# Optimization experiments

Hardware: AMD Instinct MI355X
Metric: run time of the kernel (lower is better)

Reference implementation:

```python
import jax, jax.numpy as jnp
import numpy as np
from jax import lax

B, D, H = 32768, 128, 256
N_ITER = 20


def setup_inputs() -> dict:
    key = jax.random.key(0)
    ks = jax.random.split(key, 7)
    return {
        "r": jax.random.normal(ks[0], (B, D), dtype=jnp.float32),
        "s": jax.random.normal(ks[1], (B, 1), dtype=jnp.float32),
        "pivot": jax.random.normal(ks[2], (D,), dtype=jnp.float32),
        "W1": jax.random.normal(ks[3], (D, H), dtype=jnp.float32) * 0.1,
        "b1": jax.random.normal(ks[4], (H,), dtype=jnp.float32) * 0.1,
        "w2": jax.random.normal(ks[5], (H,), dtype=jnp.float32) * 0.1,
        "b2": jax.random.normal(ks[6], (1,), dtype=jnp.float32) * 0.1,
        "n_iter": N_ITER,
    }


def _omega_step(x, W1, b1, w2, b2):
    # scalar implicit field omega evaluated on [B, D] points -> positive step in (0, 0.1)
    h = jnp.tanh(x @ W1 + b1)                      # [B, H]
    return 0.05 * (1.0 + jnp.tanh(h @ w2 + b2[0]))  # [B]


def reference(r, s, pivot, W1, b1, w2, b2, n_iter):
    # normalize ray directions; norm is detached in the original (stop_gradient)
    norm_of_x = jnp.linalg.norm(r, axis=1, keepdims=True)  # [B, 1]
    r_norm = r / lax.stop_gradient(norm_of_x)              # [B, D]

    # 20-step sphere-tracing-style ray marching along r_norm from pivot
    def step(alpha, _):
        x = pivot[None, :] + alpha[:, None] * r_norm       # [B, D]
        return alpha + _omega_step(x, W1, b1, w2, b2), None

    alpha0 = jnp.zeros((r.shape[0],), dtype=r.dtype)
    res_alpha, _ = lax.scan(step, alpha0, None, length=n_iter)  # [B]

    scale = jax.nn.sigmoid(s) * res_alpha[:, None]         # [B, 1]
    res_x = pivot[None, :] + scale * r_norm                # [B, D]
    return res_x
```

## Files before the change

### kernel.cpp

```cpp
#include <hip/hip_runtime.h>

#define DIM 128
#define HID 256
#define K2LE 2.885390081777927f
#define NTILES 16
#define RPW 16
#define WAVES 4
#define RPB (RPW * WAVES)
#define BFPAD 136

typedef __attribute__((ext_vector_type(8))) short bf16x8;
typedef __attribute__((ext_vector_type(4))) float f32x4;

__device__ __forceinline__ unsigned short f2bf(float f) {
    union { float f; unsigned u; } x; x.f = f;
    unsigned r = x.u + 0x7fffu + ((x.u >> 16) & 1u);
    return (unsigned short)(r >> 16);
}

__device__ __forceinline__ float sigmoid_fast(float x) {
    float t = __builtin_amdgcn_exp2f(-x * 1.4426950408889634f);
    return __builtin_amdgcn_rcpf(1.0f + t);
}

__global__ void k_prep(const float* __restrict__ pivot,
                       const float* __restrict__ W1,
                       const float* __restrict__ b1,
                       float* __restrict__ c2,
                       uint4* __restrict__ W1f) {
    const int tid = threadIdx.x;
    if (blockIdx.x == 0) {
        float a = b1[tid];
#pragma unroll 8
        for (int d = 0; d < DIM; ++d) a = fmaf(pivot[d], W1[d * HID + tid], a);
        c2[tid] = K2LE * a;
    }
    const int e  = blockIdx.x * 256 + tid;
    const int m  = e & 15;
    const int q  = (e >> 4) & 3;
    const int kk = (e >> 6) & 3;
    const int nt = e >> 8;
    const int n  = nt * 16 + m;
    const int k0 = kk * 32 + q * 8;
    unsigned w[4];
#pragma unroll
    for (int p = 0; p < 4; ++p) {
        unsigned lo = f2bf(W1[(k0 + 2 * p    ) * HID + n] * K2LE);
        unsigned hi = f2bf(W1[(k0 + 2 * p + 1) * HID + n] * K2LE);
        w[p] = lo | (hi << 16);
    }
    W1f[e] = make_uint4(w[0], w[1], w[2], w[3]);
}

__global__ __launch_bounds__(256, 2) void k_main(
    const float* __restrict__ r,
    const float* __restrict__ s,
    const float* __restrict__ pivot,
    const float* __restrict__ w2,
    const float* __restrict__ b2,
    const int* __restrict__ n_iter_p,
    const float* __restrict__ c2,
    const uint4* __restrict__ W1f,
    float* __restrict__ out)
{
    __shared__ unsigned short rnbf[RPB][BFPAD];
    __shared__ float alpha_s[WAVES][RPW];

    const int tid  = threadIdx.x;
    const int lane = tid & 63;
    const int wave = tid >> 6;
    const int m    = lane & 15;
    const int q    = lane >> 4;
    const int rowb = blockIdx.x * RPB + wave * RPW;
    const int n_iter = *n_iter_p;

    float2 rn2[RPW];
#pragma unroll 4
    for (int t = 0; t < RPW; ++t) {
        float2 v = *(const float2*)&r[(rowb + t) * DIM + lane * 2];
        float ss = v.x * v.x + v.y * v.y;
#pragma unroll
        for (int msk = 32; msk >= 1; msk >>= 1) ss += __shfl_xor(ss, msk, 64);
        float inv = __builtin_amdgcn_rsqf(ss);
        rn2[t].x = v.x * inv; rn2[t].y = v.y * inv;
        unsigned pack = (unsigned)f2bf(rn2[t].x) | ((unsigned)f2bf(rn2[t].y) << 16);
        *(unsigned*)&rnbf[wave * RPW + t][lane * 2] = pack;
    }

    bf16x8 afrag[4];
#pragma unroll
    for (int kk = 0; kk < 4; ++kk)
        afrag[kk] = *(const bf16x8*)&rnbf[wave * RPW + m][kk * 32 + q * 8];

    const bf16x8* __restrict__ wf = (const bf16x8*)W1f;
    const int fb = q * 16 + m;
    f32x4 acc[NTILES];
#pragma unroll
    for (int nt = 0; nt < NTILES; ++nt) {
        f32x4 a = {0.f, 0.f, 0.f, 0.f};
#pragma unroll
        for (int kk = 0; kk < 4; ++kk)
            a = __builtin_amdgcn_mfma_f32_16x16x32_bf16(
                    afrag[kk], wf[nt * 256 + kk * 64 + fb], a, 0, 0, 0);
        acc[nt] = a;
    }

    float w2f[NTILES], c2f[NTILES];
#pragma unroll
    for (int nt = 0; nt < NTILES; ++nt) {
        w2f[nt] = w2[nt * 16 + m];
        c2f[nt] = c2[nt * 16 + m];
    }
    float S = 0.f;
#pragma unroll
    for (int nt = 0; nt < NTILES; ++nt) S += w2f[nt];
#pragma unroll
    for (int msk = 1; msk <= 8; msk <<= 1) S += __shfl_xor(S, msk, 64);
    const float C0 = K2LE * (S + b2[0]);

    float alpha[4] = {0.f, 0.f, 0.f, 0.f};
    for (int it = 0; it < n_iter; ++it) {
        float part0 = 0.f, part1 = 0.f, part2 = 0.f, part3 = 0.f;
#pragma unroll
        for (int nt = 0; nt < NTILES; ++nt) {
            float u0 = __builtin_amdgcn_rcpf(__builtin_amdgcn_exp2f(fmaf(alpha[0], acc[nt][0], c2f[nt])) + 1.0f);
            float u1 = __builtin_amdgcn_rcpf(__builtin_amdgcn_exp2f(fmaf(alpha[1], acc[nt][1], c2f[nt])) + 1.0f);
            float u2 = __builtin_amdgcn_rcpf(__builtin_amdgcn_exp2f(fmaf(alpha[2], acc[nt][2], c2f[nt])) + 1.0f);
            float u3 = __builtin_amdgcn_rcpf(__builtin_amdgcn_exp2f(fmaf(alpha[3], acc[nt][3], c2f[nt])) + 1.0f);
            part0 = fmaf(w2f[nt], u0, part0);
            part1 = fmaf(w2f[nt], u1, part1);
            part2 = fmaf(w2f[nt], u2, part2);
            part3 = fmaf(w2f[nt], u3, part3);
        }
#pragma unroll
        for (int msk = 1; msk <= 8; msk <<= 1) {
            part0 += __shfl_xor(part0, msk, 64);
            part1 += __shfl_xor(part1, msk, 64);
            part2 += __shfl_xor(part2, msk, 64);
            part3 += __shfl_xor(part3, msk, 64);
        }
        float v0 = __builtin_amdgcn_rcpf(__builtin_amdgcn_exp2f(fmaf(-2.0f * K2LE, part0, C0)) + 1.0f);
        float v1 = __builtin_amdgcn_rcpf(__builtin_amdgcn_exp2f(fmaf(-2.0f * K2LE, part1, C0)) + 1.0f);
        float v2 = __builtin_amdgcn_rcpf(__builtin_amdgcn_exp2f(fmaf(-2.0f * K2LE, part2, C0)) + 1.0f);
        float v3 = __builtin_amdgcn_rcpf(__builtin_amdgcn_exp2f(fmaf(-2.0f * K2LE, part3, C0)) + 1.0f);
        alpha[0] += fmaf(-0.1f, v0, 0.1f);
        alpha[1] += fmaf(-0.1f, v1, 0.1f);
        alpha[2] += fmaf(-0.1f, v2, 0.1f);
        alpha[3] += fmaf(-0.1f, v3, 0.1f);
    }

    if (m == 0) {
#pragma unroll
        for (int rr = 0; rr < 4; ++rr) alpha_s[wave][q * 4 + rr] = alpha[rr];
    }
    __syncthreads();

    const float2 pv = *(const float2*)&pivot[lane * 2];
#pragma unroll 4
    for (int t = 0; t < RPW; ++t) {
        const int row = rowb + t;
        const float scale = sigmoid_fast(s[row]) * alpha_s[wave][t];
        float2 o;
        o.x = fmaf(scale, rn2[t].x, pv.x);
        o.y = fmaf(scale, rn2[t].y, pv.y);
        *(float2*)&out[row * DIM + lane * 2] = o;
    }
}

extern "C" void kernel_launch(void* const* d_in, const int* in_sizes, int n_in,
                              void* d_out, int out_size, void* d_ws, size_t ws_size,
                              hipStream_t stream) {
    const float* r      = (const float*)d_in[0];
    const float* s      = (const float*)d_in[1];
    const float* pivot  = (const float*)d_in[2];
    const float* W1     = (const float*)d_in[3];
    const float* b1     = (const float*)d_in[4];
    const float* w2     = (const float*)d_in[5];
    const float* b2     = (const float*)d_in[6];
    const int*   n_iter = (const int*)d_in[7];
    float* out = (float*)d_out;

    float* c2  = (float*)d_ws;
    uint4* W1f = (uint4*)((char*)d_ws + 4096);

    const int B = in_sizes[0] / DIM;

    k_prep<<<16, 256, 0, stream>>>(pivot, W1, b1, c2, W1f);
    k_main<<<B / RPB, 256, 0, stream>>>(r, s, pivot, w2, b2, n_iter, c2, W1f, out);
}
```

Measured before the change: 137.1 us.

## Split each 16-row tile across two waves to halve per-wave iteration work

Blocks now handle 32 rows instead of 64. Each pair of waves computes the same 16x256 MFMA tile, and each wave keeps only two of the four accumulator rows for the 20-step march. The normalized rays move from registers into a float LDS buffer, and launch bounds rise to 4 blocks per CU. The aim is to cut register pressure and the serial transcendental chain per wave, raising occupancy and latency hiding. The cost is duplicated MFMA work, extra LDS traffic and an added barrier.

New measurement: 137.5 us. No clear change (+0.2%).

```diff
diff --git a/kernel.cpp b/kernel.cpp
--- a/kernel.cpp
+++ b/kernel.cpp
@@ -4,9 +4,7 @@
 #define HID 256
 #define K2LE 2.885390081777927f
 #define NTILES 16
-#define RPW 16
-#define WAVES 4
-#define RPB (RPW * WAVES)
+#define RPB 32
 #define BFPAD 136
 
 typedef __attribute__((ext_vector_type(8))) short bf16x8;
@@ -52,7 +50,7 @@
     W1f[e] = make_uint4(w[0], w[1], w[2], w[3]);
 }
 
-__global__ __launch_bounds__(256, 2) void k_main(
+__global__ __launch_bounds__(256, 4) void k_main(
     const float* __restrict__ r,
     const float* __restrict__ s,
     const float* __restrict__ pivot,
@@ -64,37 +62,42 @@
     float* __restrict__ out)
 {
     __shared__ unsigned short rnbf[RPB][BFPAD];
-    __shared__ float alpha_s[WAVES][RPW];
+    __shared__ float rnf[RPB][DIM];
+    __shared__ float alpha_s[RPB];
 
     const int tid  = threadIdx.x;
     const int lane = tid & 63;
     const int wave = tid >> 6;
+    const int pr   = wave >> 1;
+    const int par  = wave & 1;
     const int m    = lane & 15;
     const int q    = lane >> 4;
-    const int rowb = blockIdx.x * RPB + wave * RPW;
+    const int rowblk = blockIdx.x * RPB;
     const int n_iter = *n_iter_p;
 
-    float2 rn2[RPW];
-#pragma unroll 4
-    for (int t = 0; t < RPW; ++t) {
-        float2 v = *(const float2*)&r[(rowb + t) * DIM + lane * 2];
+#pragma unroll
+    for (int t = 0; t < 8; ++t) {
+        const int lr = wave * 8 + t;
+        float2 v = *(const float2*)&r[(rowblk + lr) * DIM + lane * 2];
         float ss = v.x * v.x + v.y * v.y;
 #pragma unroll
         for (int msk = 32; msk >= 1; msk >>= 1) ss += __shfl_xor(ss, msk, 64);
         float inv = __builtin_amdgcn_rsqf(ss);
-        rn2[t].x = v.x * inv; rn2[t].y = v.y * inv;
-        unsigned pack = (unsigned)f2bf(rn2[t].x) | ((unsigned)f2bf(rn2[t].y) << 16);
-        *(unsigned*)&rnbf[wave * RPW + t][lane * 2] = pack;
+        float2 rn; rn.x = v.x * inv; rn.y = v.y * inv;
+        *(float2*)&rnf[lr][lane * 2] = rn;
+        unsigned pack = (unsigned)f2bf(rn.x) | ((unsigned)f2bf(rn.y) << 16);
+        *(unsigned*)&rnbf[lr][lane * 2] = pack;
     }
+    __syncthreads();
 
     bf16x8 afrag[4];
 #pragma unroll
     for (int kk = 0; kk < 4; ++kk)
-        afrag[kk] = *(const bf16x8*)&rnbf[wave * RPW + m][kk * 32 + q * 8];
+        afrag[kk] = *(const bf16x8*)&rnbf[pr * 16 + m][kk * 32 + q * 8];
 
     const bf16x8* __restrict__ wf = (const bf16x8*)W1f;
     const int fb = q * 16 + m;
-    f32x4 acc[NTILES];
+    float gA[NTILES], gB[NTILES];
 #pragma unroll
     for (int nt = 0; nt < NTILES; ++nt) {
         f32x4 a = {0.f, 0.f, 0.f, 0.f};
@@ -102,7 +105,8 @@
         for (int kk = 0; kk < 4; ++kk)
             a = __builtin_amdgcn_mfma_f32_16x16x32_bf16(
                     afrag[kk], wf[nt * 256 + kk * 64 + fb], a, 0, 0, 0);
-        acc[nt] = a;
+        gA[nt] = a[par * 2 + 0];
+        gB[nt] = a[par * 2 + 1];
     }
 
     float w2f[NTILES], c2f[NTILES];
@@ -118,51 +122,43 @@
     for (int msk = 1; msk <= 8; msk <<= 1) S += __shfl_xor(S, msk, 64);
     const float C0 = K2LE * (S + b2[0]);
 
-    float alpha[4] = {0.f, 0.f, 0.f, 0.f};
+    float alphaA = 0.f, alphaB = 0.f;
     for (int it = 0; it < n_iter; ++it) {
-        float part0 = 0.f, part1 = 0.f, part2 = 0.f, part3 = 0.f;
+        float pA = 0.f, pB = 0.f;
 #pragma unroll
         for (int nt = 0; nt < NTILES; ++nt) {
-            float u0 = __builtin_amdgcn_rcpf(__builtin_amdgcn_exp2f(fmaf(alpha[0], acc[nt][0], c2f[nt])) + 1.0f);
-            float u1 = __builtin_amdgcn_rcpf(__builtin_amdgcn_exp2f(fmaf(alpha[1], acc[nt][1], c2f[nt])) + 1.0f);
-            float u2 = __builtin_amdgcn_rcpf(__builtin_amdgcn_exp2f(fmaf(alpha[2], acc[nt][2], c2f[nt])) + 1.0f);
-            float u3 = __builtin_amdgcn_rcpf(__builtin_amdgcn_exp2f(fmaf(alpha[3], acc[nt][3], c2f[nt])) + 1.0f);
-            part0 = fmaf(w2f[nt], u0, part0);
-            part1 = fmaf(w2f[nt], u1, part1);
-            part2 = fmaf(w2f[nt], u2, part2);
-            part3 = fmaf(w2f[nt], u3, part3);
+            float uA = __builtin_amdgcn_rcpf(__builtin_amdgcn_exp2f(fmaf(alphaA, gA[nt], c2f[nt])) + 1.0f);
+            float uB = __builtin_amdgcn_rcpf(__builtin_amdgcn_exp2f(fmaf(alphaB, gB[nt], c2f[nt])) + 1.0f);
+            pA = fmaf(w2f[nt], uA, pA);
+            pB = fmaf(w2f[nt], uB, pB);
         }
 #pragma unroll
         for (int msk = 1; msk <= 8; msk <<= 1) {
-            part0 += __shfl_xor(part0, msk, 64);
-            part1 += __shfl_xor(part1, msk, 64);
-            part2 += __shfl_xor(part2, msk, 64);
-            part3 += __shfl_xor(part3, msk, 64);
+            pA += __shfl_xor(pA, msk, 64);
+            pB += __shfl_xor(pB, msk, 64);
         }
-        float v0 = __builtin_amdgcn_rcpf(__builtin_amdgcn_exp2f(fmaf(-2.0f * K2LE, part0, C0)) + 1.0f);
-        float v1 = __builtin_amdgcn_rcpf(__builtin_amdgcn_exp2f(fmaf(-2.0f * K2LE, part1, C0)) + 1.0f);
-        float v2 = __builtin_amdgcn_rcpf(__builtin_amdgcn_exp2f(fmaf(-2.0f * K2LE, part2, C0)) + 1.0f);
-        float v3 = __builtin_amdgcn_rcpf(__builtin_amdgcn_exp2f(fmaf(-2.0f * K2LE, part3, C0)) + 1.0f);
-        alpha[0] += fmaf(-0.1f, v0, 0.1f);
-        alpha[1] += fmaf(-0.1f, v1, 0.1f);
-        alpha[2] += fmaf(-0.1f, v2, 0.1f);
-        alpha[3] += fmaf(-0.1f, v3, 0.1f);
+        float vA = __builtin_amdgcn_rcpf(__builtin_amdgcn_exp2f(fmaf(-2.0f * K2LE, pA, C0)) + 1.0f);
+        float vB = __builtin_amdgcn_rcpf(__builtin_amdgcn_exp2f(fmaf(-2.0f * K2LE, pB, C0)) + 1.0f);
+        alphaA += fmaf(-0.1f, vA, 0.1f);
+        alphaB += fmaf(-0.1f, vB, 0.1f);
     }
 
     if (m == 0) {
-#pragma unroll
-        for (int rr = 0; rr < 4; ++rr) alpha_s[wave][q * 4 + rr] = alpha[rr];
+        alpha_s[pr * 16 + q * 4 + par * 2 + 0] = alphaA;
+        alpha_s[pr * 16 + q * 4 + par * 2 + 1] = alphaB;
     }
     __syncthreads();
 
     const float2 pv = *(const float2*)&pivot[lane * 2];
-#pragma unroll 4
-    for (int t = 0; t < RPW; ++t) {
-        const int row = rowb + t;
-        const float scale = sigmoid_fast(s[row]) * alpha_s[wave][t];
+#pragma unroll
+    for (int t = 0; t < 8; ++t) {
+        const int lr  = wave * 8 + t;
+        const int row = rowblk + lr;
+        const float scale = sigmoid_fast(s[row]) * alpha_s[lr];
+        float2 rn = *(const float2*)&rnf[lr][lane * 2];
         float2 o;
-        o.x = fmaf(scale, rn2[t].x, pv.x);
-        o.y = fmaf(scale, rn2[t].y, pv.y);
+        o.x = fmaf(scale, rn.x, pv.x);
+        o.y = fmaf(scale, rn.y, pv.y);
         *(float2*)&out[row * DIM + lane * 2] = o;
     }
 }
```
